# Optimization experiments

Measured on AMD Instinct MI355X. Metric: run time of the kernel, lower is better.

## Reference

```python
import jax, jax.numpy as jnp
import numpy as np

BETA = 0.9
THRESHOLD = 1.0
ATAN_ALPHA = 2.0  # snntorch ATan surrogate default


def setup_inputs() -> dict:
    key = jax.random.key(0)
    k1, k2 = jax.random.split(key)
    T, B, NI, NO = 100, 128, 2048, 1024
    x = jax.random.normal(k1, (T, B, NI), dtype=jnp.float32)
    # Kaiming-uniform-ish init like nn.Linear
    bound = 1.0 / np.sqrt(NI)
    W = jax.random.uniform(k2, (NO, NI), dtype=jnp.float32, minval=-bound, maxval=bound)
    return {"x": x, "W": W}


def _heaviside(u):
    return (u > 0).astype(u.dtype)


def reference(x, W):
    # cur[t] = x[t] @ W.T for all timesteps at once: [T, B, NO]
    cur = jnp.einsum('tbi,oi->tbo', x, W)

    def step(mem, cur_t):
        # snntorch Leaky (reset_mechanism='subtract'):
        #   reset = heaviside(mem_prev - threshold)   (detached)
        #   mem   = beta * mem_prev + cur - reset * threshold
        #   spk   = heaviside(mem - threshold)
        reset = _heaviside(mem - THRESHOLD)
        mem_new = BETA * mem + cur_t - reset * THRESHOLD
        spk = _heaviside(mem_new - THRESHOLD)
        return mem_new, (spk, mem_new)

    mem0 = jnp.zeros(cur.shape[1:], dtype=cur.dtype)  # [B, NO]
    _, (spk_rec, mem_rec) = jax.lax.scan(step, mem0, cur)
    return spk_rec, mem_rec
```

## Files before the change

### kernel.cpp

```cpp
#include <hip/hip_runtime.h>

#define T_STEPS 100
#define BATCH   128
#define NI      2048
#define NO      1024
#define M_TOT   (T_STEPS * BATCH)
#define TOTAL   (T_STEPS * BATCH * NO)
#define BNTOT   (BATCH * NO)
#define X_ELEMS (M_TOT * NI)

#define BMf 64
#define BNf 128
#define BKf 32
#define LDA (BMf + 4)
#define LDB (BNf + 4)

__global__ __launch_bounds__(256) void gemm_512fold(const float* __restrict__ X,
                                                    const float* __restrict__ W,
                                                    float* __restrict__ curOut) {
    __shared__ float As[BKf][LDA];
    __shared__ float Bs[BKf][LDB];

    const int tid = threadIdx.x;
    const int tx  = tid & 15;
    const int ty  = tid >> 4;
    const int m0  = blockIdx.y * BMf;
    const int n0  = blockIdx.x * BNf;

    const int ar = tid >> 2;
    const int ak = (tid & 3) * 4;
    const int br = tid >> 1;
    const int bk = (tid & 1) * 4;

    float ch[4][8]  = {};
    float tot[4][8] = {};

    #pragma unroll 1
    for (int k0 = 0; k0 < NI; k0 += BKf) {
        if (k0 == 512 || k0 == 1024 || k0 == 1536) {
            #pragma unroll
            for (int i = 0; i < 4; ++i)
                #pragma unroll
                for (int j = 0; j < 8; ++j) {
                    tot[i][j] = __fadd_rn(tot[i][j], ch[i][j]);
                    ch[i][j]  = 0.0f;
                }
        }

        {
            const float4 fa0 = *reinterpret_cast<const float4*>(
                &X[(size_t)(m0 + ar) * NI + k0 + ak]);
            const float4 fa1 = *reinterpret_cast<const float4*>(
                &X[(size_t)(m0 + ar) * NI + k0 + ak + 16]);
            As[ak + 0][ar] = fa0.x;  As[ak + 1][ar] = fa0.y;
            As[ak + 2][ar] = fa0.z;  As[ak + 3][ar] = fa0.w;
            As[ak + 16][ar] = fa1.x; As[ak + 17][ar] = fa1.y;
            As[ak + 18][ar] = fa1.z; As[ak + 19][ar] = fa1.w;
            #pragma unroll
            for (int q = 0; q < 4; ++q) {
                const int kb = bk + q * 8;
                const float4 fb = *reinterpret_cast<const float4*>(
                    &W[(size_t)(n0 + br) * NI + k0 + kb]);
                Bs[kb + 0][br] = fb.x; Bs[kb + 1][br] = fb.y;
                Bs[kb + 2][br] = fb.z; Bs[kb + 3][br] = fb.w;
            }
        }
        __syncthreads();

        #pragma unroll
        for (int kk = 0; kk < BKf; ++kk) {
            float a[4], b[8];
            *reinterpret_cast<float4*>(&a[0]) =
                *reinterpret_cast<const float4*>(&As[kk][ty * 4]);
            *reinterpret_cast<float4*>(&b[0]) =
                *reinterpret_cast<const float4*>(&Bs[kk][tx * 4]);
            *reinterpret_cast<float4*>(&b[4]) =
                *reinterpret_cast<const float4*>(&Bs[kk][64 + tx * 4]);
            #pragma unroll
            for (int i = 0; i < 4; ++i)
                #pragma unroll
                for (int j = 0; j < 8; ++j)
                    ch[i][j] = __fmaf_rn(a[i], b[j], ch[i][j]);
        }
        __syncthreads();
    }

    #pragma unroll
    for (int i = 0; i < 4; ++i) {
        const size_t rowbase = (size_t)(m0 + ty * 4 + i) * NO + n0;
        #pragma unroll
        for (int h = 0; h < 2; ++h) {
            float4 v;
            v.x = __fadd_rn(tot[i][h * 4 + 0], ch[i][h * 4 + 0]);
            v.y = __fadd_rn(tot[i][h * 4 + 1], ch[i][h * 4 + 1]);
            v.z = __fadd_rn(tot[i][h * 4 + 2], ch[i][h * 4 + 2]);
            v.w = __fadd_rn(tot[i][h * 4 + 3], ch[i][h * 4 + 3]);
            *reinterpret_cast<float4*>(&curOut[rowbase + h * 64 + tx * 4]) = v;
        }
    }
}

__global__ __launch_bounds__(256) void lif_scan(float* __restrict__ spk,
                                                float* __restrict__ memf) {
    const int idx = (blockIdx.x * blockDim.x + threadIdx.x) * 4;
    float4 mem = make_float4(0.f, 0.f, 0.f, 0.f);
    for (int t = 0; t < T_STEPS; ++t) {
        const size_t i = (size_t)t * BNTOT + idx;
        const float4 cur = *reinterpret_cast<const float4*>(&memf[i]);
        float4 spkv;
        #define STEP(c)                                                   \
        {                                                                 \
            const float reset = (mem.c > 1.0f) ? 1.0f : 0.0f;             \
            float tmp = __fmul_rn(0.9f, mem.c);                           \
            tmp = __fadd_rn(tmp, cur.c);                                  \
            mem.c = __fsub_rn(tmp, reset);                                \
            spkv.c = (mem.c > 1.0f) ? 1.0f : 0.0f;                        \
        }
        STEP(x) STEP(y) STEP(z) STEP(w)
        #undef STEP
        *reinterpret_cast<float4*>(&spk[i])  = spkv;
        *reinterpret_cast<float4*>(&memf[i]) = mem;
    }
}

extern "C" void kernel_launch(void* const* d_in, const int* in_sizes, int n_in,
                              void* d_out, int out_size, void* d_ws, size_t ws_size,
                              hipStream_t stream) {
    const float* X;
    const float* W;
    if (in_sizes[0] == X_ELEMS) { X = (const float*)d_in[0]; W = (const float*)d_in[1]; }
    else                        { X = (const float*)d_in[1]; W = (const float*)d_in[0]; }

    float* spk  = (float*)d_out;
    float* memf = spk + TOTAL;

    dim3 gg(NO / BNf, M_TOT / BMf);
    gemm_512fold<<<gg, 256, 0, stream>>>(X, W, memf);

    lif_scan<<<BNTOT / 4 / 256, 256, 0, stream>>>(spk, memf);
}
```

Baseline: 721.3 us.

## Double-buffer GEMM shared-memory tiles with register prefetch of next K slab

Splits the K loop into 16-wide slabs held in two shared-memory buffers. The next slab's global loads go into registers before the current slab's FMAs and are stored to the other buffer afterwards, so only one barrier per slab is needed. This aims to hide global-memory latency behind compute and cut barrier count per K element, at the cost of more registers and smaller slabs, which mean more loop iterations. The 512-wide partial-sum folding is kept at the same K boundaries.

```diff
diff --git a/kernel.cpp b/kernel.cpp
--- a/kernel.cpp
+++ b/kernel.cpp
@@ -11,15 +11,16 @@
 
 #define BMf 64
 #define BNf 128
-#define BKf 32
+#define BKs 16
+#define NSLAB (NI / BKs)
 #define LDA (BMf + 4)
 #define LDB (BNf + 4)
 
 __global__ __launch_bounds__(256) void gemm_512fold(const float* __restrict__ X,
                                                     const float* __restrict__ W,
                                                     float* __restrict__ curOut) {
-    __shared__ float As[BKf][LDA];
-    __shared__ float Bs[BKf][LDB];
+    __shared__ float As[2][BKs][LDA];
+    __shared__ float Bs[2][BKs][LDB];
 
     const int tid = threadIdx.x;
     const int tx  = tid & 15;
@@ -30,14 +31,37 @@
     const int ar = tid >> 2;
     const int ak = (tid & 3) * 4;
     const int br = tid >> 1;
-    const int bk = (tid & 1) * 4;
+    const int bk = (tid & 1) * 8;
+
+    const float* Xp = &X[(size_t)(m0 + ar) * NI + ak];
+    const float* Wp = &W[(size_t)(n0 + br) * NI + bk];
 
     float ch[4][8]  = {};
     float tot[4][8] = {};
 
+    float4 pa  = *reinterpret_cast<const float4*>(&Xp[0]);
+    float4 pb0 = *reinterpret_cast<const float4*>(&Wp[0]);
+    float4 pb1 = *reinterpret_cast<const float4*>(&Wp[4]);
+    As[0][ak + 0][ar] = pa.x;  As[0][ak + 1][ar] = pa.y;
+    As[0][ak + 2][ar] = pa.z;  As[0][ak + 3][ar] = pa.w;
+    Bs[0][bk + 0][br] = pb0.x; Bs[0][bk + 1][br] = pb0.y;
+    Bs[0][bk + 2][br] = pb0.z; Bs[0][bk + 3][br] = pb0.w;
+    Bs[0][bk + 4][br] = pb1.x; Bs[0][bk + 5][br] = pb1.y;
+    Bs[0][bk + 6][br] = pb1.z; Bs[0][bk + 7][br] = pb1.w;
+    __syncthreads();
+
     #pragma unroll 1
-    for (int k0 = 0; k0 < NI; k0 += BKf) {
-        if (k0 == 512 || k0 == 1024 || k0 == 1536) {
+    for (int s = 0; s < NSLAB; ++s) {
+        const int p = s & 1;
+
+        if (s < NSLAB - 1) {
+            const int kn = (s + 1) * BKs;
+            pa  = *reinterpret_cast<const float4*>(&Xp[kn]);
+            pb0 = *reinterpret_cast<const float4*>(&Wp[kn]);
+            pb1 = *reinterpret_cast<const float4*>(&Wp[kn + 4]);
+        }
+
+        if (s == 32 || s == 64 || s == 96) {
             #pragma unroll
             for (int i = 0; i < 4; ++i)
                 #pragma unroll
@@ -47,42 +71,32 @@
                 }
         }
 
-        {
-            const float4 fa0 = *reinterpret_cast<const float4*>(
-                &X[(size_t)(m0 + ar) * NI + k0 + ak]);
-            const float4 fa1 = *reinterpret_cast<const float4*>(
-                &X[(size_t)(m0 + ar) * NI + k0 + ak + 16]);
-            As[ak + 0][ar] = fa0.x;  As[ak + 1][ar] = fa0.y;
-            As[ak + 2][ar] = fa0.z;  As[ak + 3][ar] = fa0.w;
-            As[ak + 16][ar] = fa1.x; As[ak + 17][ar] = fa1.y;
-            As[ak + 18][ar] = fa1.z; As[ak + 19][ar] = fa1.w;
-            #pragma unroll
-            for (int q = 0; q < 4; ++q) {
-                const int kb = bk + q * 8;
-                const float4 fb = *reinterpret_cast<const float4*>(
-                    &W[(size_t)(n0 + br) * NI + k0 + kb]);
-                Bs[kb + 0][br] = fb.x; Bs[kb + 1][br] = fb.y;
-                Bs[kb + 2][br] = fb.z; Bs[kb + 3][br] = fb.w;
-            }
-        }
-        __syncthreads();
-
         #pragma unroll
-        for (int kk = 0; kk < BKf; ++kk) {
+        for (int kk = 0; kk < BKs; ++kk) {
             float a[4], b[8];
             *reinterpret_cast<float4*>(&a[0]) =
-                *reinterpret_cast<const float4*>(&As[kk][ty * 4]);
+                *reinterpret_cast<const float4*>(&As[p][kk][ty * 4]);
             *reinterpret_cast<float4*>(&b[0]) =
-                *reinterpret_cast<const float4*>(&Bs[kk][tx * 4]);
+                *reinterpret_cast<const float4*>(&Bs[p][kk][tx * 4]);
             *reinterpret_cast<float4*>(&b[4]) =
-                *reinterpret_cast<const float4*>(&Bs[kk][64 + tx * 4]);
+                *reinterpret_cast<const float4*>(&Bs[p][kk][64 + tx * 4]);
             #pragma unroll
             for (int i = 0; i < 4; ++i)
                 #pragma unroll
                 for (int j = 0; j < 8; ++j)
                     ch[i][j] = __fmaf_rn(a[i], b[j], ch[i][j]);
         }
-        __syncthreads();
+
+        if (s < NSLAB - 1) {
+            const int q = p ^ 1;
+            As[q][ak + 0][ar] = pa.x;  As[q][ak + 1][ar] = pa.y;
+            As[q][ak + 2][ar] = pa.z;  As[q][ak + 3][ar] = pa.w;
+            Bs[q][bk + 0][br] = pb0.x; Bs[q][bk + 1][br] = pb0.y;
+            Bs[q][bk + 2][br] = pb0.z; Bs[q][bk + 3][br] = pb0.w;
+            Bs[q][bk + 4][br] = pb1.x; Bs[q][bk + 5][br] = pb1.y;
+            Bs[q][bk + 6][br] = pb1.z; Bs[q][bk + 7][br] = pb1.w;
+            __syncthreads();
+        }
     }
 
     #pragma unroll
```

Measured after the change: 1.044 ms. 1.45x slower.
